# Performance work log

Measured on AMD Instinct MI355X. Metric: run time of the kernel, lower is better.

The kernel has to match this reference:

```python
import jax, jax.numpy as jnp
import numpy as np

N = 8192
IN_F = 512
OUT_F = 256


def mish(x):
    return x * jnp.tanh(jax.nn.softplus(x))


def setup_inputs() -> dict:
    key = jax.random.key(0)
    k1, k2, k3, k4 = jax.random.split(key, 4)
    inp = jax.random.normal(k1, (N, IN_F), dtype=jnp.float32)
    # random binary adjacency mask (float, used via adj > 0), ensure self-loops
    adj = jax.random.randint(k2, (N, N), 0, 2).astype(jnp.float32)
    adj = adj.at[jnp.arange(N), jnp.arange(N)].set(1.0)
    # xavier_uniform_ init
    lim_W = float(np.sqrt(6.0 / (IN_F + OUT_F)))
    W = jax.random.uniform(k3, (IN_F, OUT_F), minval=-lim_W, maxval=lim_W, dtype=jnp.float32)
    lim_a = float(np.sqrt(6.0 / (2 * OUT_F + 1)))
    a = jax.random.uniform(k4, (2 * OUT_F, 1), minval=-lim_a, maxval=lim_a, dtype=jnp.float32)
    return {"input": inp, "adj": adj, "W": W, "a": a}


def reference(input, adj, W, a):
    # h: [N, F_out]
    h = input @ W
    f_out = W.shape[1]
    a1 = a[:f_out, 0]   # applied to source node (row i)
    a2 = a[f_out:, 0]   # applied to target node (col j)
    # e[i, j] = mish(h_i . a1 + h_j . a2)  -- identical math to the
    # O(N^2*2F) concat([h_i, h_j]) @ a in the torch reference.
    e = mish((h @ a1)[:, None] + (h @ a2)[None, :])  # [N, N]
    attention = jnp.where(adj > 0, e, jnp.float32(-9e15))
    attention = jax.nn.softmax(attention, axis=1)
    # dropout is inference-off (training=False)
    h_prime = attention @ h  # [N, F_out]
    return mish(h_prime)
```

## Files before the change

### kernel.cpp

```cpp
#include <hip/hip_runtime.h>

typedef __attribute__((ext_vector_type(8))) short short8;
typedef __attribute__((ext_vector_type(4))) float f32x4;

#define L2E 1.44269504088896340736f

__device__ __forceinline__ unsigned short f2bf(float x) {
    union { float f; unsigned int u; } v; v.f = x;
    unsigned int u = v.u;
    unsigned int r = (u + 0x7FFFu + ((u >> 16) & 1u)) >> 16;
    return (unsigned short)r;
}

__device__ __forceinline__ float expw(float x) {
    float u = __builtin_amdgcn_exp2f(x * L2E);
    float t = u * (u + 2.0f);
    float m = x * t * __builtin_amdgcn_rcpf(t + 2.0f);
    return __builtin_amdgcn_exp2f(m * L2E);
}

__device__ __forceinline__ float mishf(float x) {
    float u = __builtin_amdgcn_exp2f(x * L2E);
    float t = u * (u + 2.0f);
    return x * t * __builtin_amdgcn_rcpf(t + 2.0f);
}

__global__ void k_cvt_wt(const float* __restrict__ W, unsigned short* __restrict__ wt) {
    int c = blockIdx.x;
    int t = threadIdx.x;
    wt[c * 512 + t]       = f2bf(W[(size_t)t * 256 + c]);
    wt[c * 512 + t + 256] = f2bf(W[(size_t)(t + 256) * 256 + c]);
}

__global__ __launch_bounds__(128) void k_gemm_h(const float* __restrict__ input,
                                                const unsigned short* __restrict__ wt,
                                                float* __restrict__ h,
                                                unsigned short* __restrict__ hbt) {
    int tid = threadIdx.x;
    int w = tid >> 6, lane = tid & 63, g = lane >> 4, r = lane & 15;
    int base = blockIdx.x * 32 + w * 16;

    f32x4 acc[16];
#pragma unroll
    for (int n = 0; n < 16; ++n) acc[n] = (f32x4)0.0f;

    const float* arow = input + (size_t)(base + r) * 512 + g * 8;
    for (int kb = 0; kb < 512; kb += 32) {
        float4 a0 = *(const float4*)(arow + kb);
        float4 a1 = *(const float4*)(arow + kb + 4);
        short8 af;
        af[0] = (short)f2bf(a0.x); af[1] = (short)f2bf(a0.y);
        af[2] = (short)f2bf(a0.z); af[3] = (short)f2bf(a0.w);
        af[4] = (short)f2bf(a1.x); af[5] = (short)f2bf(a1.y);
        af[6] = (short)f2bf(a1.z); af[7] = (short)f2bf(a1.w);
#pragma unroll
        for (int n = 0; n < 16; ++n) {
            short8 bf = *(const short8*)(wt + (size_t)(n * 16 + r) * 512 + kb + g * 8);
            acc[n] = __builtin_amdgcn_mfma_f32_16x16x32_bf16(af, bf, acc[n], 0, 0, 0);
        }
    }
    int rowc = base + g * 4;
#pragma unroll
    for (int n = 0; n < 16; ++n) {
        int col = n * 16 + r;
#pragma unroll
        for (int i = 0; i < 4; ++i)
            h[(size_t)(rowc + i) * 256 + col] = acc[n][i];
        ushort4 pk;
        pk.x = f2bf(acc[n][0]); pk.y = f2bf(acc[n][1]);
        pk.z = f2bf(acc[n][2]); pk.w = f2bf(acc[n][3]);
        *(ushort4*)(hbt + (size_t)col * 8192 + rowc) = pk;
    }
}

__global__ void k_s1s2(const float* __restrict__ h, const float* __restrict__ a,
                       float* __restrict__ s1, float* __restrict__ s2) {
    int lane = threadIdx.x & 63;
    int i = blockIdx.x * 4 + (threadIdx.x >> 6);
    const float* hr = h + (size_t)i * 256;
    float p1 = 0.f, p2 = 0.f;
#pragma unroll
    for (int q = 0; q < 4; ++q) {
        int f = lane + q * 64;
        float hv = hr[f];
        p1 += hv * a[f];
        p2 += hv * a[256 + f];
    }
#pragma unroll
    for (int off = 32; off >= 1; off >>= 1) {
        p1 += __shfl_xor(p1, off);
        p2 += __shfl_xor(p2, off);
    }
    if (lane == 0) { s1[i] = p1; s2[i] = p2; }
}

__global__ __launch_bounds__(512, 1) void k_attn(const float* __restrict__ adj,
                                                 const unsigned short* __restrict__ hbt,
                                                 const float* __restrict__ s1,
                                                 const float* __restrict__ s2,
                                                 float* __restrict__ pS,
                                                 float* __restrict__ pZ) {
    __shared__ __align__(16) unsigned short tile[2][8192];

    int tid = threadIdx.x;
    int w = tid >> 6, lane = tid & 63, g = lane >> 4, r = lane & 15;
    int mb = blockIdx.x, chunk = blockIdx.y;
    int rowA = mb * 128 + w * 16 + r;
    const float* adjrow = adj + (size_t)rowA * 8192;
    float s1v = s1[rowA];

    int c0 = tid, c1 = tid + 512;
    int row0 = c0 >> 2, sl0 = c0 & 3;
    int row1 = c1 >> 2, sl1 = c1 & 3;
    int ss0 = sl0 ^ ((row0 >> 1) & 3);
    int ss1 = sl1 ^ ((row1 >> 1) & 3);
    const unsigned short* hp0 = hbt + (size_t)row0 * 8192 + ss0 * 8;
    const unsigned short* hp1 = hbt + (size_t)row1 * 8192 + ss1 * 8;
    int ld0 = row0 * 32 + sl0 * 8, ld1 = row1 * 32 + sl1 * 8;
    int kc = chunk * 2048;
    int sw = (r >> 1) & 3;
    int boff = r * 32 + ((g ^ sw) * 8);
    const float* s2g = s2 + g * 8;

    f32x4 acc[17];
#pragma unroll
    for (int n = 0; n < 17; ++n) acc[n] = (f32x4)0.0f;

    short8 onef;
    {
        short ov = (r == 0) ? (short)0x3F80 : (short)0;
#pragma unroll
        for (int j = 0; j < 8; ++j) onef[j] = ov;
    }

    {
        uint4 st0 = *(const uint4*)(hp0 + kc);
        uint4 st1 = *(const uint4*)(hp1 + kc);
        *(uint4*)&tile[0][ld0] = st0;
        *(uint4*)&tile[0][ld1] = st1;
    }
    float4 aj0 = *(const float4*)(adjrow + kc + g * 8);
    float4 aj1 = *(const float4*)(adjrow + kc + g * 8 + 4);
    float4 sv0 = *(const float4*)(s2g + kc);
    float4 sv1 = *(const float4*)(s2g + kc + 4);
    __syncthreads();

    for (int s = 0; s < 64; ++s) {
        int b = s & 1;
        int kn = kc + ((s < 63) ? (s + 1) * 32 : 0);
        uint4 nt0 = *(const uint4*)(hp0 + kn);
        uint4 nt1 = *(const uint4*)(hp1 + kn);
        float4 na0 = *(const float4*)(adjrow + kn + g * 8);
        float4 na1 = *(const float4*)(adjrow + kn + g * 8 + 4);
        float4 nv0 = *(const float4*)(s2g + kn);
        float4 nv1 = *(const float4*)(s2g + kn + 4);

        short8 af;
        af[0] = (short)f2bf(aj0.x * expw(s1v + sv0.x));
        af[1] = (short)f2bf(aj0.y * expw(s1v + sv0.y));
        af[2] = (short)f2bf(aj0.z * expw(s1v + sv0.z));
        af[3] = (short)f2bf(aj0.w * expw(s1v + sv0.w));
        af[4] = (short)f2bf(aj1.x * expw(s1v + sv1.x));
        af[5] = (short)f2bf(aj1.y * expw(s1v + sv1.y));
        af[6] = (short)f2bf(aj1.z * expw(s1v + sv1.z));
        af[7] = (short)f2bf(aj1.w * expw(s1v + sv1.w));

        const unsigned short* tb = &tile[b][boff];
#pragma unroll
        for (int n = 0; n < 16; ++n) {
            short8 bf = *(const short8*)(tb + n * 512);
            acc[n] = __builtin_amdgcn_mfma_f32_16x16x32_bf16(af, bf, acc[n], 0, 0, 0);
        }
        acc[16] = __builtin_amdgcn_mfma_f32_16x16x32_bf16(af, onef, acc[16], 0, 0, 0);

        __syncthreads();
        *(uint4*)&tile[b ^ 1][ld0] = nt0;
        *(uint4*)&tile[b ^ 1][ld1] = nt1;
        aj0 = na0; aj1 = na1; sv0 = nv0; sv1 = nv1;
        __syncthreads();
    }

    float* ps = pS + ((size_t)chunk << 21);
    int rowc = mb * 128 + w * 16 + g * 4;
#pragma unroll
    for (int n = 0; n < 16; ++n) {
#pragma unroll
        for (int i = 0; i < 4; ++i)
            ps[(size_t)(rowc + i) * 256 + n * 16 + r] = acc[n][i];
    }
    if (r == 0) {
        float* pz = pZ + chunk * 8192 + rowc;
#pragma unroll
        for (int i = 0; i < 4; ++i) pz[i] = acc[16][i];
    }
}

__global__ void k_final(const float* __restrict__ pS, const float* __restrict__ pZ,
                        float* __restrict__ out) {
    int i = blockIdx.x;
    int f = threadIdx.x;
    size_t o = (size_t)i * 256 + f;
    float sv = pS[o] + pS[o + (1u << 21)] + pS[o + (2u << 21)] + pS[o + (3u << 21)];
    float z = pZ[i] + pZ[i + 8192] + pZ[i + 16384] + pZ[i + 24576];
    float hp = sv / z;
    out[o] = mishf(hp);
}

extern "C" void kernel_launch(void* const* d_in, const int* in_sizes, int n_in,
                              void* d_out, int out_size, void* d_ws, size_t ws_size,
                              hipStream_t stream) {
    const float* input = (const float*)d_in[0];
    const float* adj   = (const float*)d_in[1];
    const float* W     = (const float*)d_in[2];
    const float* a     = (const float*)d_in[3];
    float* out = (float*)d_out;

    char* ws = (char*)d_ws;
    unsigned short* wt  = (unsigned short*)ws;
    float*  h   = (float*)(ws + 262144);
    unsigned short* hbt = (unsigned short*)(ws + 8650752);
    float*  s1  = (float*)(ws + 12845056);
    float*  s2  = (float*)(ws + 12877824);
    float*  pS  = (float*)(ws + 12910592);
    float*  pZ  = (float*)(ws + 46465024);

    hipLaunchKernelGGL(k_cvt_wt, dim3(256), dim3(256), 0, stream, W, wt);
    hipLaunchKernelGGL(k_gemm_h, dim3(256), dim3(128), 0, stream, input, wt, h, hbt);
    hipLaunchKernelGGL(k_s1s2, dim3(2048), dim3(256), 0, stream, h, a, s1, s2);
    hipLaunchKernelGGL(k_attn, dim3(64, 4), dim3(512), 0, stream, adj, hbt, s1, s2, pS, pZ);
    hipLaunchKernelGGL(k_final, dim3(8192), dim3(256), 0, stream, pS, pZ, out);
}
```

Baseline: 511.4 us.

## Fuse score dot-products into GEMM, triple-buffer attention with direct-to-LDS loads

The s1/s2 dot-product kernel is folded into the h GEMM epilogue, which also drops the fp32 h store and precomputes log2-scaled scores and exp2(s2). The attention kernel now uses 256-thread blocks at two blocks per CU. It keeps a three-stage LDS ring filled by global_load_lds, with one barrier per step in place of two and a manual vmcnt wait. The exponent is factored so only one exp2 per element remains, and rounding to bf16 is simplified. The cost is an extra e2 load stream and a more fragile hand-tuned wait count.

```diff
diff --git a/kernel.cpp b/kernel.cpp
--- a/kernel.cpp
+++ b/kernel.cpp
@@ -12,17 +12,26 @@
     return (unsigned short)r;
 }
 
-__device__ __forceinline__ float expw(float x) {
-    float u = __builtin_amdgcn_exp2f(x * L2E);
-    float t = u * (u + 2.0f);
-    float m = x * t * __builtin_amdgcn_rcpf(t + 2.0f);
-    return __builtin_amdgcn_exp2f(m * L2E);
-}
-
 __device__ __forceinline__ float mishf(float x) {
     float u = __builtin_amdgcn_exp2f(x * L2E);
     float t = u * (u + 2.0f);
     return x * t * __builtin_amdgcn_rcpf(t + 2.0f);
+}
+
+__device__ __forceinline__ short pw(float aj, float sv, float ev, float s1Lv, float e1v) {
+    float xL = s1Lv + sv;
+    float u  = e1v * ev;
+    float t  = u * (u + 2.0f);
+    float m  = xL * t * __builtin_amdgcn_rcpf(t + 2.0f);
+    float p  = aj * __builtin_amdgcn_exp2f(m);
+    union { float f; unsigned int u; } b; b.f = p;
+    return (short)((b.u + 0x8000u) >> 16);
+}
+
+typedef __attribute__((address_space(1))) const unsigned int guint;
+typedef __attribute__((address_space(3))) unsigned int luint;
+__device__ __forceinline__ void lds16(const void* g, void* l) {
+    __builtin_amdgcn_global_load_lds((guint*)g, (luint*)l, 16, 0, 0);
 }
 
 __global__ void k_cvt_wt(const float* __restrict__ W, unsigned short* __restrict__ wt) {
@@ -32,19 +41,22 @@
     wt[c * 512 + t + 256] = f2bf(W[(size_t)(t + 256) * 256 + c]);
 }
 
-__global__ __launch_bounds__(128) void k_gemm_h(const float* __restrict__ input,
-                                                const unsigned short* __restrict__ wt,
-                                                float* __restrict__ h,
-                                                unsigned short* __restrict__ hbt) {
-    int tid = threadIdx.x;
-    int w = tid >> 6, lane = tid & 63, g = lane >> 4, r = lane & 15;
-    int base = blockIdx.x * 32 + w * 16;
+__global__ __launch_bounds__(64) void k_gemm_h(const float* __restrict__ input,
+                                               const unsigned short* __restrict__ wt,
+                                               const float* __restrict__ a,
+                                               unsigned short* __restrict__ hbt,
+                                               float* __restrict__ s1L,
+                                               float* __restrict__ s2L,
+                                               float* __restrict__ e2) {
+    int lane = threadIdx.x & 63, g = lane >> 4, r = lane & 15;
+    int base = blockIdx.x * 16;
 
     f32x4 acc[16];
 #pragma unroll
     for (int n = 0; n < 16; ++n) acc[n] = (f32x4)0.0f;
 
     const float* arow = input + (size_t)(base + r) * 512 + g * 8;
+#pragma unroll 2
     for (int kb = 0; kb < 512; kb += 32) {
         float4 a0 = *(const float4*)(arow + kb);
         float4 a1 = *(const float4*)(arow + kb + 4);
@@ -63,64 +75,78 @@
 #pragma unroll
     for (int n = 0; n < 16; ++n) {
         int col = n * 16 + r;
-#pragma unroll
-        for (int i = 0; i < 4; ++i)
-            h[(size_t)(rowc + i) * 256 + col] = acc[n][i];
         ushort4 pk;
         pk.x = f2bf(acc[n][0]); pk.y = f2bf(acc[n][1]);
         pk.z = f2bf(acc[n][2]); pk.w = f2bf(acc[n][3]);
         *(ushort4*)(hbt + (size_t)col * 8192 + rowc) = pk;
     }
-}
-
-__global__ void k_s1s2(const float* __restrict__ h, const float* __restrict__ a,
-                       float* __restrict__ s1, float* __restrict__ s2) {
-    int lane = threadIdx.x & 63;
-    int i = blockIdx.x * 4 + (threadIdx.x >> 6);
-    const float* hr = h + (size_t)i * 256;
-    float p1 = 0.f, p2 = 0.f;
-#pragma unroll
-    for (int q = 0; q < 4; ++q) {
-        int f = lane + q * 64;
-        float hv = hr[f];
-        p1 += hv * a[f];
-        p2 += hv * a[256 + f];
-    }
-#pragma unroll
-    for (int off = 32; off >= 1; off >>= 1) {
-        p1 += __shfl_xor(p1, off);
-        p2 += __shfl_xor(p2, off);
-    }
-    if (lane == 0) { s1[i] = p1; s2[i] = p2; }
-}
-
-__global__ __launch_bounds__(512, 1) void k_attn(const float* __restrict__ adj,
+    float p1[4] = {0,0,0,0}, p2[4] = {0,0,0,0};
+#pragma unroll
+    for (int n = 0; n < 16; ++n) {
+        float a1v = a[n * 16 + r];
+        float a2v = a[256 + n * 16 + r];
+#pragma unroll
+        for (int i = 0; i < 4; ++i) {
+            p1[i] += acc[n][i] * a1v;
+            p2[i] += acc[n][i] * a2v;
+        }
+    }
+#pragma unroll
+    for (int off = 8; off >= 1; off >>= 1) {
+#pragma unroll
+        for (int i = 0; i < 4; ++i) {
+            p1[i] += __shfl_xor(p1[i], off);
+            p2[i] += __shfl_xor(p2[i], off);
+        }
+    }
+    if (r == 0) {
+#pragma unroll
+        for (int i = 0; i < 4; ++i) {
+            int row = rowc + i;
+            s1L[row] = p1[i] * L2E;
+            float s2l = p2[i] * L2E;
+            s2L[row] = s2l;
+            e2[row] = __builtin_amdgcn_exp2f(s2l);
+        }
+    }
+}
+
+__global__ __launch_bounds__(256, 2) void k_attn(const float* __restrict__ adj,
                                                  const unsigned short* __restrict__ hbt,
-                                                 const float* __restrict__ s1,
-                                                 const float* __restrict__ s2,
+                                                 const float* __restrict__ s1L,
+                                                 const float* __restrict__ s2L,
+                                                 const float* __restrict__ e2,
                                                  float* __restrict__ pS,
                                                  float* __restrict__ pZ) {
-    __shared__ __align__(16) unsigned short tile[2][8192];
+    __shared__ __align__(16) unsigned short tile[3][8192];
 
     int tid = threadIdx.x;
     int w = tid >> 6, lane = tid & 63, g = lane >> 4, r = lane & 15;
     int mb = blockIdx.x, chunk = blockIdx.y;
-    int rowA = mb * 128 + w * 16 + r;
-    const float* adjrow = adj + (size_t)rowA * 8192;
-    float s1v = s1[rowA];
-
-    int c0 = tid, c1 = tid + 512;
-    int row0 = c0 >> 2, sl0 = c0 & 3;
-    int row1 = c1 >> 2, sl1 = c1 & 3;
-    int ss0 = sl0 ^ ((row0 >> 1) & 3);
-    int ss1 = sl1 ^ ((row1 >> 1) & 3);
-    const unsigned short* hp0 = hbt + (size_t)row0 * 8192 + ss0 * 8;
-    const unsigned short* hp1 = hbt + (size_t)row1 * 8192 + ss1 * 8;
-    int ld0 = row0 * 32 + sl0 * 8, ld1 = row1 * 32 + sl1 * 8;
     int kc = chunk * 2048;
+    int rowA = mb * 64 + w * 16 + r;
+    float s1Lv = s1L[rowA];
+    float e1v = __builtin_amdgcn_exp2f(s1Lv);
+
+    const float* adjp = adj + (size_t)rowA * 8192 + kc + g * 8;
+    const float* svp  = s2L + kc + g * 8;
+    const float* evp  = e2  + kc + g * 8;
+
+    const unsigned short *hsrc0, *hsrc1, *hsrc2, *hsrc3;
+    {
+        int l2 = lane >> 2, sl = lane & 3;
+        int r0 = 64 * w + l2,      ss0 = sl ^ ((r0 >> 1) & 3);
+        int r1 = 64 * w + 16 + l2, ss1 = sl ^ ((r1 >> 1) & 3);
+        int r2 = 64 * w + 32 + l2, ss2 = sl ^ ((r2 >> 1) & 3);
+        int r3 = 64 * w + 48 + l2, ss3 = sl ^ ((r3 >> 1) & 3);
+        hsrc0 = hbt + (size_t)r0 * 8192 + kc + ss0 * 8;
+        hsrc1 = hbt + (size_t)r1 * 8192 + kc + ss1 * 8;
+        hsrc2 = hbt + (size_t)r2 * 8192 + kc + ss2 * 8;
+        hsrc3 = hbt + (size_t)r3 * 8192 + kc + ss3 * 8;
+    }
+    char* ldsbase = (char*)&tile[0][0] + w * 4096;
     int sw = (r >> 1) & 3;
-    int boff = r * 32 + ((g ^ sw) * 8);
-    const float* s2g = s2 + g * 8;
+    int rdoff = r * 64 + ((g ^ sw) * 16);
 
     f32x4 acc[17];
 #pragma unroll
@@ -133,55 +159,68 @@
         for (int j = 0; j < 8; ++j) onef[j] = ov;
     }
 
-    {
-        uint4 st0 = *(const uint4*)(hp0 + kc);
-        uint4 st1 = *(const uint4*)(hp1 + kc);
-        *(uint4*)&tile[0][ld0] = st0;
-        *(uint4*)&tile[0][ld1] = st1;
-    }
-    float4 aj0 = *(const float4*)(adjrow + kc + g * 8);
-    float4 aj1 = *(const float4*)(adjrow + kc + g * 8 + 4);
-    float4 sv0 = *(const float4*)(s2g + kc);
-    float4 sv1 = *(const float4*)(s2g + kc + 4);
-    __syncthreads();
-
-    for (int s = 0; s < 64; ++s) {
-        int b = s & 1;
-        int kn = kc + ((s < 63) ? (s + 1) * 32 : 0);
-        uint4 nt0 = *(const uint4*)(hp0 + kn);
-        uint4 nt1 = *(const uint4*)(hp1 + kn);
-        float4 na0 = *(const float4*)(adjrow + kn + g * 8);
-        float4 na1 = *(const float4*)(adjrow + kn + g * 8 + 4);
-        float4 nv0 = *(const float4*)(s2g + kn);
-        float4 nv1 = *(const float4*)(s2g + kn + 4);
-
-        short8 af;
-        af[0] = (short)f2bf(aj0.x * expw(s1v + sv0.x));
-        af[1] = (short)f2bf(aj0.y * expw(s1v + sv0.y));
-        af[2] = (short)f2bf(aj0.z * expw(s1v + sv0.z));
-        af[3] = (short)f2bf(aj0.w * expw(s1v + sv0.w));
-        af[4] = (short)f2bf(aj1.x * expw(s1v + sv1.x));
-        af[5] = (short)f2bf(aj1.y * expw(s1v + sv1.y));
-        af[6] = (short)f2bf(aj1.z * expw(s1v + sv1.z));
-        af[7] = (short)f2bf(aj1.w * expw(s1v + sv1.w));
-
-        const unsigned short* tb = &tile[b][boff];
-#pragma unroll
-        for (int n = 0; n < 16; ++n) {
-            short8 bf = *(const short8*)(tb + n * 512);
-            acc[n] = __builtin_amdgcn_mfma_f32_16x16x32_bf16(af, bf, acc[n], 0, 0, 0);
-        }
-        acc[16] = __builtin_amdgcn_mfma_f32_16x16x32_bf16(af, onef, acc[16], 0, 0, 0);
-
-        __syncthreads();
-        *(uint4*)&tile[b ^ 1][ld0] = nt0;
-        *(uint4*)&tile[b ^ 1][ld1] = nt1;
-        aj0 = na0; aj1 = na1; sv0 = nv0; sv1 = nv1;
-        __syncthreads();
+    float4 ajA0, ajA1, svA0, svA1, evA0, evA1;
+    float4 ajB0, ajB1, svB0, svB1, evB0, evB1;
+
+#define ISSUE(tt, bufn, AJ0, AJ1, SV0, SV1, EV0, EV1) do {                     \
+        int t_ = (tt); if (t_ > 63) t_ = 63;                                   \
+        int ko_ = t_ * 32;                                                     \
+        char* lb_ = ldsbase + (bufn) * 16384;                                  \
+        lds16(hsrc0 + ko_, lb_);                                               \
+        lds16(hsrc1 + ko_, lb_ + 1024);                                        \
+        lds16(hsrc2 + ko_, lb_ + 2048);                                        \
+        lds16(hsrc3 + ko_, lb_ + 3072);                                        \
+        AJ0 = *(const float4*)(adjp + ko_);                                    \
+        AJ1 = *(const float4*)(adjp + ko_ + 4);                                \
+        SV0 = *(const float4*)(svp + ko_);                                     \
+        SV1 = *(const float4*)(svp + ko_ + 4);                                 \
+        EV0 = *(const float4*)(evp + ko_);                                     \
+        EV1 = *(const float4*)(evp + ko_ + 4);                                 \
+    } while (0)
+
+#define WAITBAR() do {                                                         \
+        asm volatile("s_waitcnt vmcnt(10)" ::: "memory");                      \
+        __builtin_amdgcn_sched_barrier(0);                                     \
+        __builtin_amdgcn_s_barrier();                                          \
+        __builtin_amdgcn_sched_barrier(0);                                     \
+    } while (0)
+
+#define COMPUTE(bufc, AJ0, AJ1, SV0, SV1, EV0, EV1) do {                       \
+        short8 af_;                                                            \
+        af_[0] = pw(AJ0.x, SV0.x, EV0.x, s1Lv, e1v);                           \
+        af_[1] = pw(AJ0.y, SV0.y, EV0.y, s1Lv, e1v);                           \
+        af_[2] = pw(AJ0.z, SV0.z, EV0.z, s1Lv, e1v);                           \
+        af_[3] = pw(AJ0.w, SV0.w, EV0.w, s1Lv, e1v);                           \
+        af_[4] = pw(AJ1.x, SV1.x, EV1.x, s1Lv, e1v);                           \
+        af_[5] = pw(AJ1.y, SV1.y, EV1.y, s1Lv, e1v);                           \
+        af_[6] = pw(AJ1.z, SV1.z, EV1.z, s1Lv, e1v);                           \
+        af_[7] = pw(AJ1.w, SV1.w, EV1.w, s1Lv, e1v);                           \
+        const char* tb_ = (const char*)&tile[0][0] + (bufc) * 16384 + rdoff;   \
+        _Pragma("unroll")                                                      \
+        for (int n_ = 0; n_ < 16; ++n_) {                                      \
+            short8 bf_ = *(const short8*)(tb_ + n_ * 1024);                    \
+            acc[n_] = __builtin_amdgcn_mfma_f32_16x16x32_bf16(af_, bf_, acc[n_], 0, 0, 0); \
+        }                                                                      \
+        acc[16] = __builtin_amdgcn_mfma_f32_16x16x32_bf16(af_, onef, acc[16], 0, 0, 0);    \
+    } while (0)
+
+    ISSUE(0, 0, ajA0, ajA1, svA0, svA1, evA0, evA1);
+
+    int cur = 0;
+    for (int s = 0; s < 64; s += 2) {
+        int nb = cur + 1; if (nb == 3) nb = 0;
+        ISSUE(s + 1, nb, ajB0, ajB1, svB0, svB1, evB0, evB1);
+        WAITBAR();
+        COMPUTE(cur, ajA0, ajA1, svA0, svA1, evA0, evA1);
+        cur = nb; nb = cur + 1; if (nb == 3) nb = 0;
+        ISSUE(s + 2, nb, ajA0, ajA1, svA0, svA1, evA0, evA1);
+        WAITBAR();
+        COMPUTE(cur, ajB0, ajB1, svB0, svB1, evB0, evB1);
+        cur = nb;
     }
 
     float* ps = pS + ((size_t)chunk << 21);
-    int rowc = mb * 128 + w * 16 + g * 4;
+    int rowc = mb * 64 + w * 16 + g * 4;
 #pragma unroll
     for (int n = 0; n < 16; ++n) {
 #pragma unroll
@@ -193,6 +232,9 @@
 #pragma unroll
         for (int i = 0; i < 4; ++i) pz[i] = acc[16][i];
     }
+#undef ISSUE
+#undef WAITBAR
+#undef COMPUTE
 }
 
 __global__ void k_final(const float* __restrict__ pS, const float* __restrict__ pZ,
@@ -217,16 +259,15 @@
 
     char* ws = (char*)d_ws;
     unsigned short* wt  = (unsigned short*)ws;
-    float*  h   = (float*)(ws + 262144);
-    unsigned short* hbt = (unsigned short*)(ws + 8650752);
-    float*  s1  = (float*)(ws + 12845056);
-    float*  s2  = (float*)(ws + 12877824);
-    float*  pS  = (float*)(ws + 12910592);
-    float*  pZ  = (float*)(ws + 46465024);
+    unsigned short* hbt = (unsigned short*)(ws + 262144);
+    float* s1L = (float*)(ws + 4456448);
+    float* s2L = (float*)(ws + 4489216);
+    float* e2  = (float*)(ws + 4521984);
+    float* pS  = (float*)(ws + 4554752);
+    float* pZ  = (float*)(ws + 38109184);
 
     hipLaunchKernelGGL(k_cvt_wt, dim3(256), dim3(256), 0, stream, W, wt);
-    hipLaunchKernelGGL(k_gemm_h, dim3(256), dim3(128), 0, stream, input, wt, h, hbt);
-    hipLaunchKernelGGL(k_s1s2, dim3(2048), dim3(256), 0, stream, h, a, s1, s2);
-    hipLaunchKernelGGL(k_attn, dim3(64, 4), dim3(512), 0, stream, adj, hbt, s1, s2, pS, pZ);
+    hipLaunchKernelGGL(k_gemm_h, dim3(512), dim3(64), 0, stream, input, wt, a, hbt, s1L, s2L, e2);
+    hipLaunchKernelGGL(k_attn, dim3(128, 4), dim3(256), 0, stream, adj, hbt, s1L, s2L, e2, pS, pZ);
     hipLaunchKernelGGL(k_final, dim3(8192), dim3(256), 0, stream, pS, pZ, out);
 }
```

Result: faster. 460.1 us (-10.0%).
